# Performance work log

Hardware: AMD Instinct MI355X
Metric: run time of the kernel (lower is better)

## Reference

```python
import jax, jax.numpy as jnp
import numpy as np

ARITY, LABEL_DIM, H_DIM, B = 2, 128, 512, 16384
ARG_DIM = LABEL_DIM + ARITY * H_DIM


def setup_inputs() -> dict:
    key = jax.random.key(0)
    ks = jax.random.split(key, 12)
    s_lin = 1.0 / np.sqrt(ARG_DIM)
    inp = {
        "label": jax.random.normal(ks[0], (B, LABEL_DIM), jnp.float32),
        "children_h": jax.random.normal(ks[1], (ARITY, B, H_DIM), jnp.float32),
        "children_c": jax.random.normal(ks[2], (ARITY, B, H_DIM), jnp.float32),
        # torch Linear params: W (h, arg_dim), b (h,)
        "W_i": jax.random.normal(ks[3], (H_DIM, ARG_DIM), jnp.float32) * s_lin,
        "b_i": jax.random.normal(ks[4], (H_DIM,), jnp.float32) * s_lin,
        "W_o": jax.random.normal(ks[5], (H_DIM, ARG_DIM), jnp.float32) * s_lin,
        "b_o": jax.random.normal(ks[6], (H_DIM,), jnp.float32) * s_lin,
        "W_u": jax.random.normal(ks[7], (H_DIM, ARG_DIM), jnp.float32) * s_lin,
        "b_u": jax.random.normal(ks[8], (H_DIM,), jnp.float32) * s_lin,
        # forget params (xavier-ish init)
        "W_fl": jax.random.normal(ks[9], (H_DIM, LABEL_DIM), jnp.float32) * np.sqrt(2.0 / (H_DIM + LABEL_DIM)),
        "W_fs": jax.random.normal(ks[10], (ARITY, ARITY, H_DIM, H_DIM), jnp.float32) * np.sqrt(1.0 / H_DIM),
        "forget_bias": jax.random.normal(ks[11], (H_DIM,), jnp.float32) * 0.1,
    }
    return inp


def reference(label, children_h, children_c, W_i, b_i, W_o, b_o, W_u, b_u, W_fl, W_fs, forget_bias):
    arity, b, h = children_h.shape
    # x = cat([label, h_0, ..., h_{arity-1}], dim=1)  -> (B, arg_dim)
    x = jnp.concatenate([label, children_h.transpose(1, 0, 2).reshape(b, arity * h)], axis=1)
    i_gate = jax.nn.sigmoid(x @ W_i.T + b_i)
    o_gate = jax.nn.sigmoid(x @ W_o.T + b_o)
    u = jnp.tanh(x @ W_u.T + b_u)
    # per-child forget weight: [W_fl | W_fs[k,0] | ... | W_fs[k,arity-1]]  -> (arity, h, arg_dim)
    Wf = jnp.concatenate(
        [jnp.broadcast_to(W_fl, (arity,) + W_fl.shape),
         W_fs.transpose(0, 2, 1, 3).reshape(arity, h, arity * h)],
        axis=2,
    )
    # bmm (no bias inside sigmoid; forget_bias enters separately below)
    f = jax.nn.sigmoid(jnp.einsum("khd,bd->kbh", Wf, x))
    cells_composed = (f * children_c).sum(axis=0)          # (B, h)
    cells_forget_bias = forget_bias * children_c.sum(axis=0)
    next_cell = i_gate * u + cells_composed + cells_forget_bias
    out = jnp.tanh(o_gate * next_cell)
    return (next_cell, out)
```

## Files before the change

kernel.cpp:

```cpp
#include <hip/hip_runtime.h>
#include <hip/hip_bf16.h>
#include <cstdint>
#include <cstddef>

#define BROWS   16384
#define LDIM    128
#define HDIM    512
#define KDIM    1152
#define NGATES  2560
#define NKT     (KDIM / 64)

#define XB_BYTES  ((size_t)BROWS * KDIM * 2)
#define WB_BYTES  ((size_t)NGATES * KDIM * 2)

using f32x4   = __attribute__((ext_vector_type(4))) float;
using bfrag   = __attribute__((ext_vector_type(8))) short;

__device__ __forceinline__ short f2bf(float f) {
    union { float f; uint32_t u; } a; a.f = f;
    uint32_t u = a.u;
    uint32_t lsb = (u >> 16) & 1u;
    u += 0x7fffu + lsb;
    return (short)(u >> 16);
}
__device__ __forceinline__ float bf2f(short s) {
    union { uint32_t u; float f; } a;
    a.u = ((uint32_t)(uint16_t)s) << 16;
    return a.f;
}

__device__ __forceinline__ void load_lds16(const void* g, void* l) {
    __builtin_amdgcn_global_load_lds(
        (const __attribute__((address_space(1))) void*)g,
        (__attribute__((address_space(3))) void*)l, 16, 0, 0);
}

__device__ __forceinline__ float fast_sigmoid(float x) {
    return 1.0f / (1.0f + __expf(-x));
}
__device__ __forceinline__ float fast_tanh(float x) {
    float t = __expf(2.0f * x);
    return 1.0f - 2.0f / (t + 1.0f);
}

#define NBX  ((BROWS  * (KDIM / 8)) / 256)
#define NBW  ((NGATES * (KDIM / 8)) / 256)

__global__ __launch_bounds__(256) void pack_all(
    const float* __restrict__ label, const float* __restrict__ chh,
    const float* __restrict__ Wi, const float* __restrict__ Wo,
    const float* __restrict__ Wu, const float* __restrict__ Wfl,
    const float* __restrict__ Wfs,
    short* __restrict__ xb, short* __restrict__ Wb)
{
    const int perRow = KDIM / 8;
    int blk = blockIdx.x;
    const float* src;
    short* dst;
    if (blk < NBX) {
        int tid = blk * 256 + threadIdx.x;
        int b = tid / perRow;
        int d = (tid - b * perRow) * 8;
        if (d < LDIM) {
            src = label + (size_t)b * LDIM + d;
        } else {
            int dd = d - LDIM;
            int k  = dd >> 9;
            int j  = dd & 511;
            src = chh + ((size_t)k * BROWS + b) * HDIM + j;
        }
        dst = xb + (size_t)b * KDIM + d;
    } else {
        int tid = (blk - NBX) * 256 + threadIdx.x;
        int n = tid / perRow;
        int d = (tid - n * perRow) * 8;
        int g = n >> 9, h = n & 511;
        if (g == 0)      src = Wi + (size_t)h * KDIM + d;
        else if (g == 1) src = Wo + (size_t)h * KDIM + d;
        else if (g == 2) src = Wu + (size_t)h * KDIM + d;
        else {
            int k = g - 3;
            if (d < LDIM) {
                src = Wfl + (size_t)h * LDIM + d;
            } else {
                int dd = d - LDIM;
                int j  = dd >> 9;
                int jj = dd & 511;
                src = Wfs + (((size_t)(k * 2 + j) * HDIM + h) * HDIM) + jj;
            }
        }
        dst = Wb + (size_t)n * KDIM + d;
    }
    float4 v0 = *(const float4*)src;
    float4 v1 = *(const float4*)(src + 4);
    bfrag s;
    s[0] = f2bf(v0.x); s[1] = f2bf(v0.y); s[2] = f2bf(v0.z); s[3] = f2bf(v0.w);
    s[4] = f2bf(v1.x); s[5] = f2bf(v1.y); s[6] = f2bf(v1.z); s[7] = f2bf(v1.w);
    *(bfrag*)dst = s;
}

__global__ __launch_bounds__(512, 2) void gemm_bt(const short* __restrict__ A,
                                                  const short* __restrict__ Bt,
                                                  short* __restrict__ C) {
    __shared__ short As[2][16384];
    __shared__ short Bs[2][16384];

    const int t    = threadIdx.x;
    const int lane = t & 63;
    const int wave = t >> 6;
    const int wr   = wave >> 2;
    const int wc   = wave & 3;
    const int quad = lane >> 4;
    const int l16  = lane & 15;

    const int local = blockIdx.x >> 3;
    const int mT    = (blockIdx.x & 7) * 8 + local / 10;
    const int nT    = local % 10;
    const int mBase = mT * 256;
    const int nBase = nT * 256;

    f32x4 acc[8][4] = {};

    const int sr  = t >> 3;
    const int ssl = (t & 7) ^ (sr & 7);
    const short* aSrc = A  + (size_t)(mBase + sr) * KDIM + ssl * 8;
    const short* bSrc = Bt + (size_t)(nBase + sr) * KDIM + ssl * 8;
    short* aDst = &As[0][0] + t * 8;
    short* bDst = &Bs[0][0] + t * 8;

#define STAGE_A(q, kt, buf) load_lds16(aSrc + (size_t)(q) * (64 * KDIM) + (kt) * 64, \
                                       aDst + (buf) * 16384 + (q) * 4096)
#define STAGE_B(q, kt, buf) load_lds16(bSrc + (size_t)(q) * (64 * KDIM) + (kt) * 64, \
                                       bDst + (buf) * 16384 + (q) * 4096)

    const int kswz0 = ((quad)     ^ (l16 & 7)) << 4;
    const int kswz1 = ((quad + 4) ^ (l16 & 7)) << 4;
    const int aRowB = (wr * 128 + l16) << 7;
    const int bRowB = (wc * 64  + l16) << 7;

#define DS_A(buf, mh, i, ks) (*(const bfrag*)((const char*)(&As[(buf)][0]) + aRowB + \
                              (mh) * 8192 + (i) * 2048 + ((ks) ? kswz1 : kswz0)))
#define DS_B(buf, j, ks) (*(const bfrag*)((const char*)(&Bs[(buf)][0]) + bRowB + \
                              (j) * 2048 + ((ks) ? kswz1 : kswz0)))

#define MM(af, bfr, mi, ni) acc[mi][ni] = \
    __builtin_amdgcn_mfma_f32_16x16x32_bf16(af, bfr, acc[mi][ni], 0, 0, 0)

#define PHASE(buf, mh, ks, ...) do { \
    bfrag a0 = DS_A(buf, mh, 0, ks); \
    bfrag a1 = DS_A(buf, mh, 1, ks); \
    bfrag a2 = DS_A(buf, mh, 2, ks); \
    bfrag a3 = DS_A(buf, mh, 3, ks); \
    bfrag b0 = DS_B(buf, 0, ks); \
    bfrag b1 = DS_B(buf, 1, ks); \
    bfrag b2 = DS_B(buf, 2, ks); \
    bfrag b3 = DS_B(buf, 3, ks); \
    __VA_ARGS__; \
    __builtin_amdgcn_s_setprio(1); \
    MM(a0, b0, (mh)*4+0, 0); MM(a0, b1, (mh)*4+0, 1); \
    MM(a0, b2, (mh)*4+0, 2); MM(a0, b3, (mh)*4+0, 3); \
    MM(a1, b0, (mh)*4+1, 0); MM(a1, b1, (mh)*4+1, 1); \
    MM(a1, b2, (mh)*4+1, 2); MM(a1, b3, (mh)*4+1, 3); \
    MM(a2, b0, (mh)*4+2, 0); MM(a2, b1, (mh)*4+2, 1); \
    MM(a2, b2, (mh)*4+2, 2); MM(a2, b3, (mh)*4+2, 3); \
    MM(a3, b0, (mh)*4+3, 0); MM(a3, b1, (mh)*4+3, 1); \
    MM(a3, b2, (mh)*4+3, 2); MM(a3, b3, (mh)*4+3, 3); \
    __builtin_amdgcn_s_setprio(0); \
} while (0)

    STAGE_A(0, 0, 0); STAGE_A(1, 0, 0); STAGE_A(2, 0, 0); STAGE_A(3, 0, 0);
    STAGE_B(0, 0, 0); STAGE_B(1, 0, 0); STAGE_B(2, 0, 0); STAGE_B(3, 0, 0);
    STAGE_A(0, 1, 1); STAGE_A(2, 1, 1);
    asm volatile("s_waitcnt vmcnt(2)" ::: "memory");
    __builtin_amdgcn_s_barrier();

#pragma unroll 1
    for (int k2 = 0; k2 < NKT / 2; ++k2) {
        const int kt   = 2 * k2;
        const bool more = (k2 < NKT / 2 - 1);

        PHASE(0, 0, 0, STAGE_A(1, kt + 1, 1); STAGE_B(0, kt + 1, 1); STAGE_B(1, kt + 1, 1));
        __builtin_amdgcn_s_barrier();
        PHASE(0, 0, 1, STAGE_A(3, kt + 1, 1); STAGE_B(2, kt + 1, 1); STAGE_B(3, kt + 1, 1));
        __builtin_amdgcn_s_barrier();
        PHASE(0, 1, 0, if (more) STAGE_A(0, kt + 2, 0));
        __builtin_amdgcn_s_barrier();
        PHASE(0, 1, 1, if (more) STAGE_A(2, kt + 2, 0));
        if (more) { asm volatile("s_waitcnt vmcnt(2)" ::: "memory"); }
        else      { asm volatile("s_waitcnt vmcnt(0)" ::: "memory"); }
        __builtin_amdgcn_s_barrier();

        PHASE(1, 0, 0, if (more) { STAGE_A(1, kt + 2, 0); STAGE_B(0, kt + 2, 0); STAGE_B(1, kt + 2, 0); });
        __builtin_amdgcn_s_barrier();
        PHASE(1, 0, 1, if (more) { STAGE_A(3, kt + 2, 0); STAGE_B(2, kt + 2, 0); STAGE_B(3, kt + 2, 0); });
        __builtin_amdgcn_s_barrier();
        PHASE(1, 1, 0, if (more) STAGE_A(0, kt + 3, 1));
        __builtin_amdgcn_s_barrier();
        PHASE(1, 1, 1, if (more) STAGE_A(2, kt + 3, 1));
        if (more) { asm volatile("s_waitcnt vmcnt(2)" ::: "memory"); }
        else      { asm volatile("s_waitcnt vmcnt(0)" ::: "memory"); }
        __builtin_amdgcn_s_barrier();
    }

#pragma unroll
    for (int mi = 0; mi < 8; ++mi) {
        const int row0 = mBase + wr * 128 + mi * 16 + quad * 4;
#pragma unroll
        for (int ni = 0; ni < 4; ++ni) {
            const int col = nBase + wc * 64 + ni * 16 + l16;
#pragma unroll
            for (int r = 0; r < 4; ++r) {
                C[(size_t)(row0 + r) * NGATES + col] = f2bf(acc[mi][ni][r]);
            }
        }
    }
#undef PHASE
#undef MM
#undef DS_A
#undef DS_B
#undef STAGE_A
#undef STAGE_B
}

__global__ __launch_bounds__(256) void epilogue(const short* __restrict__ gates,
                                                const float* __restrict__ chc,
                                                const float* __restrict__ b_i,
                                                const float* __restrict__ b_o,
                                                const float* __restrict__ b_u,
                                                const float* __restrict__ fbias,
                                                float* __restrict__ out) {
    int tid = blockIdx.x * 256 + threadIdx.x;
    int b  = tid >> 6;
    int h8 = (tid & 63) << 3;

    const short* g = gates + (size_t)b * NGATES + h8;
    bfrag vi  = *(const bfrag*)(g);
    bfrag vo  = *(const bfrag*)(g + HDIM);
    bfrag vu  = *(const bfrag*)(g + 2 * HDIM);
    bfrag vf0 = *(const bfrag*)(g + 3 * HDIM);
    bfrag vf1 = *(const bfrag*)(g + 4 * HDIM);

    float4 bi0 = *(const float4*)(b_i + h8),   bi1 = *(const float4*)(b_i + h8 + 4);
    float4 bo0 = *(const float4*)(b_o + h8),   bo1 = *(const float4*)(b_o + h8 + 4);
    float4 bu0 = *(const float4*)(b_u + h8),   bu1 = *(const float4*)(b_u + h8 + 4);
    float4 fb0 = *(const float4*)(fbias + h8), fb1 = *(const float4*)(fbias + h8 + 4);

    size_t cbase = (size_t)b * HDIM + h8;
    float4 c00 = *(const float4*)(chc + cbase);
    float4 c01 = *(const float4*)(chc + cbase + 4);
    float4 c10 = *(const float4*)(chc + (size_t)BROWS * HDIM + cbase);
    float4 c11 = *(const float4*)(chc + (size_t)BROWS * HDIM + cbase + 4);

    float bi[8] = {bi0.x,bi0.y,bi0.z,bi0.w, bi1.x,bi1.y,bi1.z,bi1.w};
    float bo[8] = {bo0.x,bo0.y,bo0.z,bo0.w, bo1.x,bo1.y,bo1.z,bo1.w};
    float bu[8] = {bu0.x,bu0.y,bu0.z,bu0.w, bu1.x,bu1.y,bu1.z,bu1.w};
    float fb[8] = {fb0.x,fb0.y,fb0.z,fb0.w, fb1.x,fb1.y,fb1.z,fb1.w};
    float c0[8] = {c00.x,c00.y,c00.z,c00.w, c01.x,c01.y,c01.z,c01.w};
    float c1[8] = {c10.x,c10.y,c10.z,c10.w, c11.x,c11.y,c11.z,c11.w};

    float nc[8], ou[8];
#pragma unroll
    for (int e = 0; e < 8; ++e) {
        float ig = fast_sigmoid(bf2f(vi[e]) + bi[e]);
        float og = fast_sigmoid(bf2f(vo[e]) + bo[e]);
        float uu = fast_tanh(bf2f(vu[e]) + bu[e]);
        float f0 = fast_sigmoid(bf2f(vf0[e]));
        float f1 = fast_sigmoid(bf2f(vf1[e]));
        float ncell = ig * uu + f0 * c0[e] + f1 * c1[e] + fb[e] * (c0[e] + c1[e]);
        nc[e] = ncell;
        ou[e] = fast_tanh(og * ncell);
    }
    float4 n0 = {nc[0], nc[1], nc[2], nc[3]}, n1 = {nc[4], nc[5], nc[6], nc[7]};
    float4 o0 = {ou[0], ou[1], ou[2], ou[3]}, o1 = {ou[4], ou[5], ou[6], ou[7]};
    *(float4*)(out + cbase)     = n0;
    *(float4*)(out + cbase + 4) = n1;
    *(float4*)(out + (size_t)BROWS * HDIM + cbase)     = o0;
    *(float4*)(out + (size_t)BROWS * HDIM + cbase + 4) = o1;
}

extern "C" void kernel_launch(void* const* d_in, const int* in_sizes, int n_in,
                              void* d_out, int out_size, void* d_ws, size_t ws_size,
                              hipStream_t stream) {
    const float* label = (const float*)d_in[0];
    const float* chh   = (const float*)d_in[1];
    const float* chc   = (const float*)d_in[2];
    const float* W_i   = (const float*)d_in[3];
    const float* b_i   = (const float*)d_in[4];
    const float* W_o   = (const float*)d_in[5];
    const float* b_o   = (const float*)d_in[6];
    const float* W_u   = (const float*)d_in[7];
    const float* b_u   = (const float*)d_in[8];
    const float* W_fl  = (const float*)d_in[9];
    const float* W_fs  = (const float*)d_in[10];
    const float* fbias = (const float*)d_in[11];
    float* out = (float*)d_out;

    char* ws = (char*)d_ws;
    short* xb    = (short*)ws;
    short* Wb    = (short*)(ws + XB_BYTES);
    short* gates = (short*)(ws + XB_BYTES + WB_BYTES);

    pack_all<<<NBX + NBW, 256, 0, stream>>>(label, chh, W_i, W_o, W_u, W_fl, W_fs, xb, Wb);

    gemm_bt<<<dim3(640), 512, 0, stream>>>(xb, Wb, gates);

    epilogue<<<(BROWS * (HDIM / 8)) / 256, 256, 0, stream>>>(gates, chc, b_i, b_o, b_u, fbias, out);
}
```

Measured before the change: 332.2 us.

## Switch GEMM main loop to triple-buffered K=32 tiles with single barrier per tile

The bf16 GEMM main loop now uses 32-wide K tiles held in a three-stage LDS ring instead of 64-wide tiles in a double buffer. Each tile issues the prefetch two tiles ahead, loads all A/B fragments, runs 32 MFMAs, then waits and syncs once. This cuts the number of barriers per K step and deepens prefetch to hide global-load latency. The cost is more loop iterations with less MFMA work between each sync, and a different LDS swizzle pattern.

```diff
diff --git a/kernel.cpp b/kernel.cpp
--- a/kernel.cpp
+++ b/kernel.cpp
@@ -8,7 +8,7 @@
 #define HDIM    512
 #define KDIM    1152
 #define NGATES  2560
-#define NKT     (KDIM / 64)
+#define NKT32   36
 
 #define XB_BYTES  ((size_t)BROWS * KDIM * 2)
 #define WB_BYTES  ((size_t)NGATES * KDIM * 2)
@@ -102,8 +102,8 @@
 __global__ __launch_bounds__(512, 2) void gemm_bt(const short* __restrict__ A,
                                                   const short* __restrict__ Bt,
                                                   short* __restrict__ C) {
-    __shared__ short As[2][16384];
-    __shared__ short Bs[2][16384];
+    __shared__ short As[3][8192];
+    __shared__ short Bs[3][8192];
 
     const int t    = threadIdx.x;
     const int lane = t & 63;
@@ -121,100 +121,76 @@
 
     f32x4 acc[8][4] = {};
 
-    const int sr  = t >> 3;
-    const int ssl = (t & 7) ^ (sr & 7);
+    const int sr  = t >> 2;
+    const int ssl = (t & 3) ^ (sr & 3);
     const short* aSrc = A  + (size_t)(mBase + sr) * KDIM + ssl * 8;
     const short* bSrc = Bt + (size_t)(nBase + sr) * KDIM + ssl * 8;
     short* aDst = &As[0][0] + t * 8;
     short* bDst = &Bs[0][0] + t * 8;
 
-#define STAGE_A(q, kt, buf) load_lds16(aSrc + (size_t)(q) * (64 * KDIM) + (kt) * 64, \
-                                       aDst + (buf) * 16384 + (q) * 4096)
-#define STAGE_B(q, kt, buf) load_lds16(bSrc + (size_t)(q) * (64 * KDIM) + (kt) * 64, \
-                                       bDst + (buf) * 16384 + (q) * 4096)
-
-    const int kswz0 = ((quad)     ^ (l16 & 7)) << 4;
-    const int kswz1 = ((quad + 4) ^ (l16 & 7)) << 4;
-    const int aRowB = (wr * 128 + l16) << 7;
-    const int bRowB = (wc * 64  + l16) << 7;
-
-#define DS_A(buf, mh, i, ks) (*(const bfrag*)((const char*)(&As[(buf)][0]) + aRowB + \
-                              (mh) * 8192 + (i) * 2048 + ((ks) ? kswz1 : kswz0)))
-#define DS_B(buf, j, ks) (*(const bfrag*)((const char*)(&Bs[(buf)][0]) + bRowB + \
-                              (j) * 2048 + ((ks) ? kswz1 : kswz0)))
-
-#define MM(af, bfr, mi, ni) acc[mi][ni] = \
-    __builtin_amdgcn_mfma_f32_16x16x32_bf16(af, bfr, acc[mi][ni], 0, 0, 0)
-
-#define PHASE(buf, mh, ks, ...) do { \
-    bfrag a0 = DS_A(buf, mh, 0, ks); \
-    bfrag a1 = DS_A(buf, mh, 1, ks); \
-    bfrag a2 = DS_A(buf, mh, 2, ks); \
-    bfrag a3 = DS_A(buf, mh, 3, ks); \
-    bfrag b0 = DS_B(buf, 0, ks); \
-    bfrag b1 = DS_B(buf, 1, ks); \
-    bfrag b2 = DS_B(buf, 2, ks); \
-    bfrag b3 = DS_B(buf, 3, ks); \
-    __VA_ARGS__; \
+#define STAGE_A(d, kt, buf) load_lds16(aSrc + (size_t)(d) * (128 * KDIM) + (kt) * 32, \
+                                       aDst + (buf) * 8192 + (d) * 4096)
+#define STAGE_B(d, kt, buf) load_lds16(bSrc + (size_t)(d) * (128 * KDIM) + (kt) * 32, \
+                                       bDst + (buf) * 8192 + (d) * 4096)
+
+    const int kswz  = (quad ^ (l16 & 3)) << 4;
+    const int aRowB = (wr * 128 + l16) * 64;
+    const int bRowB = (wc * 64  + l16) * 64;
+
+#define DS_A(buf, i) (*(const bfrag*)((const char*)(&As[0][0]) + (buf) * 16384 + aRowB + (i) * 1024 + kswz))
+#define DS_B(buf, j) (*(const bfrag*)((const char*)(&Bs[0][0]) + (buf) * 16384 + bRowB + (j) * 1024 + kswz))
+
+#define MM(af, bfr, i, j) acc[i][j] = \
+    __builtin_amdgcn_mfma_f32_16x16x32_bf16(af, bfr, acc[i][j], 0, 0, 0)
+
+#define TILE(bufc, bufs, kt, doStage, vmZero) do { \
+    if (doStage) { STAGE_A(0, (kt) + 2, bufs); STAGE_A(1, (kt) + 2, bufs); \
+                   STAGE_B(0, (kt) + 2, bufs); STAGE_B(1, (kt) + 2, bufs); } \
+    bfrag bb[4], aa[8]; \
+    bb[0] = DS_B(bufc, 0); bb[1] = DS_B(bufc, 1); \
+    bb[2] = DS_B(bufc, 2); bb[3] = DS_B(bufc, 3); \
+    aa[0] = DS_A(bufc, 0); aa[1] = DS_A(bufc, 1); \
+    aa[2] = DS_A(bufc, 2); aa[3] = DS_A(bufc, 3); \
+    aa[4] = DS_A(bufc, 4); aa[5] = DS_A(bufc, 5); \
+    aa[6] = DS_A(bufc, 6); aa[7] = DS_A(bufc, 7); \
     __builtin_amdgcn_s_setprio(1); \
-    MM(a0, b0, (mh)*4+0, 0); MM(a0, b1, (mh)*4+0, 1); \
-    MM(a0, b2, (mh)*4+0, 2); MM(a0, b3, (mh)*4+0, 3); \
-    MM(a1, b0, (mh)*4+1, 0); MM(a1, b1, (mh)*4+1, 1); \
-    MM(a1, b2, (mh)*4+1, 2); MM(a1, b3, (mh)*4+1, 3); \
-    MM(a2, b0, (mh)*4+2, 0); MM(a2, b1, (mh)*4+2, 1); \
-    MM(a2, b2, (mh)*4+2, 2); MM(a2, b3, (mh)*4+2, 3); \
-    MM(a3, b0, (mh)*4+3, 0); MM(a3, b1, (mh)*4+3, 1); \
-    MM(a3, b2, (mh)*4+3, 2); MM(a3, b3, (mh)*4+3, 3); \
+    _Pragma("unroll") \
+    for (int i = 0; i < 8; ++i) { \
+        _Pragma("unroll") \
+        for (int j = 0; j < 4; ++j) MM(aa[i], bb[j], i, j); \
+    } \
     __builtin_amdgcn_s_setprio(0); \
+    if (vmZero) { asm volatile("s_waitcnt vmcnt(0)" ::: "memory"); } \
+    else        { asm volatile("s_waitcnt vmcnt(4)" ::: "memory"); } \
+    __builtin_amdgcn_s_barrier(); \
 } while (0)
 
-    STAGE_A(0, 0, 0); STAGE_A(1, 0, 0); STAGE_A(2, 0, 0); STAGE_A(3, 0, 0);
-    STAGE_B(0, 0, 0); STAGE_B(1, 0, 0); STAGE_B(2, 0, 0); STAGE_B(3, 0, 0);
-    STAGE_A(0, 1, 1); STAGE_A(2, 1, 1);
-    asm volatile("s_waitcnt vmcnt(2)" ::: "memory");
+    STAGE_A(0, 0, 0); STAGE_A(1, 0, 0); STAGE_B(0, 0, 0); STAGE_B(1, 0, 0);
+    STAGE_A(0, 1, 1); STAGE_A(1, 1, 1); STAGE_B(0, 1, 1); STAGE_B(1, 1, 1);
+    asm volatile("s_waitcnt vmcnt(4)" ::: "memory");
     __builtin_amdgcn_s_barrier();
 
 #pragma unroll 1
-    for (int k2 = 0; k2 < NKT / 2; ++k2) {
-        const int kt   = 2 * k2;
-        const bool more = (k2 < NKT / 2 - 1);
-
-        PHASE(0, 0, 0, STAGE_A(1, kt + 1, 1); STAGE_B(0, kt + 1, 1); STAGE_B(1, kt + 1, 1));
-        __builtin_amdgcn_s_barrier();
-        PHASE(0, 0, 1, STAGE_A(3, kt + 1, 1); STAGE_B(2, kt + 1, 1); STAGE_B(3, kt + 1, 1));
-        __builtin_amdgcn_s_barrier();
-        PHASE(0, 1, 0, if (more) STAGE_A(0, kt + 2, 0));
-        __builtin_amdgcn_s_barrier();
-        PHASE(0, 1, 1, if (more) STAGE_A(2, kt + 2, 0));
-        if (more) { asm volatile("s_waitcnt vmcnt(2)" ::: "memory"); }
-        else      { asm volatile("s_waitcnt vmcnt(0)" ::: "memory"); }
-        __builtin_amdgcn_s_barrier();
-
-        PHASE(1, 0, 0, if (more) { STAGE_A(1, kt + 2, 0); STAGE_B(0, kt + 2, 0); STAGE_B(1, kt + 2, 0); });
-        __builtin_amdgcn_s_barrier();
-        PHASE(1, 0, 1, if (more) { STAGE_A(3, kt + 2, 0); STAGE_B(2, kt + 2, 0); STAGE_B(3, kt + 2, 0); });
-        __builtin_amdgcn_s_barrier();
-        PHASE(1, 1, 0, if (more) STAGE_A(0, kt + 3, 1));
-        __builtin_amdgcn_s_barrier();
-        PHASE(1, 1, 1, if (more) STAGE_A(2, kt + 3, 1));
-        if (more) { asm volatile("s_waitcnt vmcnt(2)" ::: "memory"); }
-        else      { asm volatile("s_waitcnt vmcnt(0)" ::: "memory"); }
-        __builtin_amdgcn_s_barrier();
-    }
-
-#pragma unroll
-    for (int mi = 0; mi < 8; ++mi) {
-        const int row0 = mBase + wr * 128 + mi * 16 + quad * 4;
-#pragma unroll
-        for (int ni = 0; ni < 4; ++ni) {
-            const int col = nBase + wc * 64 + ni * 16 + l16;
+    for (int k3 = 0; k3 < NKT32 / 3; ++k3) {
+        const int kt = k3 * 3;
+        TILE(0, 2, kt,     kt + 2 <= NKT32 - 1, false);
+        TILE(1, 0, kt + 1, kt + 3 <= NKT32 - 1, kt + 1 == NKT32 - 2);
+        TILE(2, 1, kt + 2, kt + 4 <= NKT32 - 1, kt + 2 == NKT32 - 2);
+    }
+
+#pragma unroll
+    for (int i = 0; i < 8; ++i) {
+        const int row0 = mBase + wr * 128 + i * 16 + quad * 4;
+#pragma unroll
+        for (int j = 0; j < 4; ++j) {
+            const int col = nBase + wc * 64 + j * 16 + l16;
 #pragma unroll
             for (int r = 0; r < 4; ++r) {
-                C[(size_t)(row0 + r) * NGATES + col] = f2bf(acc[mi][ni][r]);
+                C[(size_t)(row0 + r) * NGATES + col] = f2bf(acc[i][j][r]);
             }
         }
     }
-#undef PHASE
+#undef TILE
 #undef MM
 #undef DS_A
 #undef DS_B
```

Result: no change. 337.1 us (+1.5%).

## Fuse LSTM gate epilogue into GEMM with per-h gate-grouped tiles

Applied to the files above, without the earlier changes.

Restructures the GEMM so each block computes all five gate columns for a 64-wide slice of hidden units, then applies the sigmoid/tanh cell update directly from accumulators. This removes the bf16 gates intermediate buffer, its global write and read, and the separate epilogue launch. In exchange LDS per block grows to hold a 320-row B tile, which may reduce occupancy. Epilogue global accesses become scalar and less coalesced.

```diff
diff --git a/kernel.cpp b/kernel.cpp
--- a/kernel.cpp
+++ b/kernel.cpp
@@ -22,11 +22,6 @@
     uint32_t lsb = (u >> 16) & 1u;
     u += 0x7fffu + lsb;
     return (short)(u >> 16);
-}
-__device__ __forceinline__ float bf2f(short s) {
-    union { uint32_t u; float f; } a;
-    a.u = ((uint32_t)(uint16_t)s) << 16;
-    return a.f;
 }
 
 __device__ __forceinline__ void load_lds16(const void* g, void* l) {
@@ -99,11 +94,15 @@
     *(bfrag*)dst = s;
 }
 
-__global__ __launch_bounds__(512, 2) void gemm_bt(const short* __restrict__ A,
-                                                  const short* __restrict__ Bt,
-                                                  short* __restrict__ C) {
+__global__ __launch_bounds__(512, 2) void gemm_fused(
+    const short* __restrict__ A, const short* __restrict__ Wb,
+    const float* __restrict__ chc,
+    const float* __restrict__ b_i, const float* __restrict__ b_o,
+    const float* __restrict__ b_u, const float* __restrict__ fbias,
+    float* __restrict__ out)
+{
     __shared__ short As[2][16384];
-    __shared__ short Bs[2][16384];
+    __shared__ short Bs[2][20480];
 
     const int t    = threadIdx.x;
     const int lane = t & 63;
@@ -114,37 +113,37 @@
     const int l16  = lane & 15;
 
     const int local = blockIdx.x >> 3;
-    const int mT    = (blockIdx.x & 7) * 8 + local / 10;
-    const int nT    = local % 10;
+    const int mT    = (blockIdx.x & 7) * 8 + (local >> 3);
+    const int nT    = local & 7;
     const int mBase = mT * 256;
-    const int nBase = nT * 256;
-
-    f32x4 acc[8][4] = {};
+    const int h0    = nT * 64;
+
+    f32x4 acc[8][5] = {};
 
     const int sr  = t >> 3;
     const int ssl = (t & 7) ^ (sr & 7);
     const short* aSrc = A  + (size_t)(mBase + sr) * KDIM + ssl * 8;
-    const short* bSrc = Bt + (size_t)(nBase + sr) * KDIM + ssl * 8;
+    const short* bSrc = Wb + (size_t)(h0    + sr) * KDIM + ssl * 8;
     short* aDst = &As[0][0] + t * 8;
     short* bDst = &Bs[0][0] + t * 8;
 
 #define STAGE_A(q, kt, buf) load_lds16(aSrc + (size_t)(q) * (64 * KDIM) + (kt) * 64, \
                                        aDst + (buf) * 16384 + (q) * 4096)
-#define STAGE_B(q, kt, buf) load_lds16(bSrc + (size_t)(q) * (64 * KDIM) + (kt) * 64, \
-                                       bDst + (buf) * 16384 + (q) * 4096)
+#define STAGE_B(d, kt, buf) load_lds16(bSrc + (size_t)(d) * (512 * KDIM) + (kt) * 64, \
+                                       bDst + (buf) * 20480 + (d) * 4096)
 
     const int kswz0 = ((quad)     ^ (l16 & 7)) << 4;
     const int kswz1 = ((quad + 4) ^ (l16 & 7)) << 4;
     const int aRowB = (wr * 128 + l16) << 7;
-    const int bRowB = (wc * 64  + l16) << 7;
-
-#define DS_A(buf, mh, i, ks) (*(const bfrag*)((const char*)(&As[(buf)][0]) + aRowB + \
-                              (mh) * 8192 + (i) * 2048 + ((ks) ? kswz1 : kswz0)))
-#define DS_B(buf, j, ks) (*(const bfrag*)((const char*)(&Bs[(buf)][0]) + bRowB + \
-                              (j) * 2048 + ((ks) ? kswz1 : kswz0)))
-
-#define MM(af, bfr, mi, ni) acc[mi][ni] = \
-    __builtin_amdgcn_mfma_f32_16x16x32_bf16(af, bfr, acc[mi][ni], 0, 0, 0)
+    const int bRowB = (wc * 16  + l16) << 7;
+
+#define DS_A(buf, mh, i, ks) (*(const bfrag*)((const char*)(&As[0][0]) + (buf) * 32768 + \
+                              aRowB + (mh) * 8192 + (i) * 2048 + ((ks) ? kswz1 : kswz0)))
+#define DS_B(buf, g, ks) (*(const bfrag*)((const char*)(&Bs[0][0]) + (buf) * 40960 + \
+                              (g) * 8192 + bRowB + ((ks) ? kswz1 : kswz0)))
+
+#define MM(af, bfr, mi, g) acc[mi][g] = \
+    __builtin_amdgcn_mfma_f32_16x16x32_bf16(af, bfr, acc[mi][g], 0, 0, 0)
 
 #define PHASE(buf, mh, ks, ...) do { \
     bfrag a0 = DS_A(buf, mh, 0, ks); \
@@ -155,21 +154,23 @@
     bfrag b1 = DS_B(buf, 1, ks); \
     bfrag b2 = DS_B(buf, 2, ks); \
     bfrag b3 = DS_B(buf, 3, ks); \
+    bfrag b4 = DS_B(buf, 4, ks); \
     __VA_ARGS__; \
     __builtin_amdgcn_s_setprio(1); \
-    MM(a0, b0, (mh)*4+0, 0); MM(a0, b1, (mh)*4+0, 1); \
-    MM(a0, b2, (mh)*4+0, 2); MM(a0, b3, (mh)*4+0, 3); \
-    MM(a1, b0, (mh)*4+1, 0); MM(a1, b1, (mh)*4+1, 1); \
-    MM(a1, b2, (mh)*4+1, 2); MM(a1, b3, (mh)*4+1, 3); \
-    MM(a2, b0, (mh)*4+2, 0); MM(a2, b1, (mh)*4+2, 1); \
-    MM(a2, b2, (mh)*4+2, 2); MM(a2, b3, (mh)*4+2, 3); \
-    MM(a3, b0, (mh)*4+3, 0); MM(a3, b1, (mh)*4+3, 1); \
-    MM(a3, b2, (mh)*4+3, 2); MM(a3, b3, (mh)*4+3, 3); \
+    MM(a0, b0, (mh)*4+0, 0); MM(a0, b1, (mh)*4+0, 1); MM(a0, b2, (mh)*4+0, 2); \
+    MM(a0, b3, (mh)*4+0, 3); MM(a0, b4, (mh)*4+0, 4); \
+    MM(a1, b0, (mh)*4+1, 0); MM(a1, b1, (mh)*4+1, 1); MM(a1, b2, (mh)*4+1, 2); \
+    MM(a1, b3, (mh)*4+1, 3); MM(a1, b4, (mh)*4+1, 4); \
+    MM(a2, b0, (mh)*4+2, 0); MM(a2, b1, (mh)*4+2, 1); MM(a2, b2, (mh)*4+2, 2); \
+    MM(a2, b3, (mh)*4+2, 3); MM(a2, b4, (mh)*4+2, 4); \
+    MM(a3, b0, (mh)*4+3, 0); MM(a3, b1, (mh)*4+3, 1); MM(a3, b2, (mh)*4+3, 2); \
+    MM(a3, b3, (mh)*4+3, 3); MM(a3, b4, (mh)*4+3, 4); \
     __builtin_amdgcn_s_setprio(0); \
 } while (0)
 
     STAGE_A(0, 0, 0); STAGE_A(1, 0, 0); STAGE_A(2, 0, 0); STAGE_A(3, 0, 0);
     STAGE_B(0, 0, 0); STAGE_B(1, 0, 0); STAGE_B(2, 0, 0); STAGE_B(3, 0, 0);
+    STAGE_B(4, 0, 0);
     STAGE_A(0, 1, 1); STAGE_A(2, 1, 1);
     asm volatile("s_waitcnt vmcnt(2)" ::: "memory");
     __builtin_amdgcn_s_barrier();
@@ -183,7 +184,7 @@
         __builtin_amdgcn_s_barrier();
         PHASE(0, 0, 1, STAGE_A(3, kt + 1, 1); STAGE_B(2, kt + 1, 1); STAGE_B(3, kt + 1, 1));
         __builtin_amdgcn_s_barrier();
-        PHASE(0, 1, 0, if (more) STAGE_A(0, kt + 2, 0));
+        PHASE(0, 1, 0, STAGE_B(4, kt + 1, 1); if (more) STAGE_A(0, kt + 2, 0));
         __builtin_amdgcn_s_barrier();
         PHASE(0, 1, 1, if (more) STAGE_A(2, kt + 2, 0));
         if (more) { asm volatile("s_waitcnt vmcnt(2)" ::: "memory"); }
@@ -194,24 +195,35 @@
         __builtin_amdgcn_s_barrier();
         PHASE(1, 0, 1, if (more) { STAGE_A(3, kt + 2, 0); STAGE_B(2, kt + 2, 0); STAGE_B(3, kt + 2, 0); });
         __builtin_amdgcn_s_barrier();
-        PHASE(1, 1, 0, if (more) STAGE_A(0, kt + 3, 1));
+        PHASE(1, 1, 0, if (more) { STAGE_B(4, kt + 2, 0); STAGE_A(0, kt + 3, 1); });
         __builtin_amdgcn_s_barrier();
         PHASE(1, 1, 1, if (more) STAGE_A(2, kt + 3, 1));
         if (more) { asm volatile("s_waitcnt vmcnt(2)" ::: "memory"); }
         else      { asm volatile("s_waitcnt vmcnt(0)" ::: "memory"); }
         __builtin_amdgcn_s_barrier();
     }
+
+    const int h = h0 + wc * 16 + l16;
+    const float bi = b_i[h], bo = b_o[h], bu = b_u[h], fb = fbias[h];
+    const float* chc1 = chc + (size_t)BROWS * HDIM;
+    float* out2 = out + (size_t)BROWS * HDIM;
 
 #pragma unroll
     for (int mi = 0; mi < 8; ++mi) {
         const int row0 = mBase + wr * 128 + mi * 16 + quad * 4;
 #pragma unroll
-        for (int ni = 0; ni < 4; ++ni) {
-            const int col = nBase + wc * 64 + ni * 16 + l16;
-#pragma unroll
-            for (int r = 0; r < 4; ++r) {
-                C[(size_t)(row0 + r) * NGATES + col] = f2bf(acc[mi][ni][r]);
-            }
+        for (int r = 0; r < 4; ++r) {
+            const size_t idx = (size_t)(row0 + r) * HDIM + h;
+            float ig = fast_sigmoid(acc[mi][0][r] + bi);
+            float og = fast_sigmoid(acc[mi][1][r] + bo);
+            float uu = fast_tanh(acc[mi][2][r] + bu);
+            float f0 = fast_sigmoid(acc[mi][3][r]);
+            float f1 = fast_sigmoid(acc[mi][4][r]);
+            float c0 = chc[idx];
+            float c1 = chc1[idx];
+            float ncell = ig * uu + f0 * c0 + f1 * c1 + fb * (c0 + c1);
+            out[idx]  = ncell;
+            out2[idx] = fast_tanh(og * ncell);
         }
     }
 #undef PHASE
@@ -220,62 +232,6 @@
 #undef DS_B
 #undef STAGE_A
 #undef STAGE_B
-}
-
-__global__ __launch_bounds__(256) void epilogue(const short* __restrict__ gates,
-                                                const float* __restrict__ chc,
-                                                const float* __restrict__ b_i,
-                                                const float* __restrict__ b_o,
-                                                const float* __restrict__ b_u,
-                                                const float* __restrict__ fbias,
-                                                float* __restrict__ out) {
-    int tid = blockIdx.x * 256 + threadIdx.x;
-    int b  = tid >> 6;
-    int h8 = (tid & 63) << 3;
-
-    const short* g = gates + (size_t)b * NGATES + h8;
-    bfrag vi  = *(const bfrag*)(g);
-    bfrag vo  = *(const bfrag*)(g + HDIM);
-    bfrag vu  = *(const bfrag*)(g + 2 * HDIM);
-    bfrag vf0 = *(const bfrag*)(g + 3 * HDIM);
-    bfrag vf1 = *(const bfrag*)(g + 4 * HDIM);
-
-    float4 bi0 = *(const float4*)(b_i + h8),   bi1 = *(const float4*)(b_i + h8 + 4);
-    float4 bo0 = *(const float4*)(b_o + h8),   bo1 = *(const float4*)(b_o + h8 + 4);
-    float4 bu0 = *(const float4*)(b_u + h8),   bu1 = *(const float4*)(b_u + h8 + 4);
-    float4 fb0 = *(const float4*)(fbias + h8), fb1 = *(const float4*)(fbias + h8 + 4);
-
-    size_t cbase = (size_t)b * HDIM + h8;
-    float4 c00 = *(const float4*)(chc + cbase);
-    float4 c01 = *(const float4*)(chc + cbase + 4);
-    float4 c10 = *(const float4*)(chc + (size_t)BROWS * HDIM + cbase);
-    float4 c11 = *(const float4*)(chc + (size_t)BROWS * HDIM + cbase + 4);
-
-    float bi[8] = {bi0.x,bi0.y,bi0.z,bi0.w, bi1.x,bi1.y,bi1.z,bi1.w};
-    float bo[8] = {bo0.x,bo0.y,bo0.z,bo0.w, bo1.x,bo1.y,bo1.z,bo1.w};
-    float bu[8] = {bu0.x,bu0.y,bu0.z,bu0.w, bu1.x,bu1.y,bu1.z,bu1.w};
-    float fb[8] = {fb0.x,fb0.y,fb0.z,fb0.w, fb1.x,fb1.y,fb1.z,fb1.w};
-    float c0[8] = {c00.x,c00.y,c00.z,c00.w, c01.x,c01.y,c01.z,c01.w};
-    float c1[8] = {c10.x,c10.y,c10.z,c10.w, c11.x,c11.y,c11.z,c11.w};
-
-    float nc[8], ou[8];
-#pragma unroll
-    for (int e = 0; e < 8; ++e) {
-        float ig = fast_sigmoid(bf2f(vi[e]) + bi[e]);
-        float og = fast_sigmoid(bf2f(vo[e]) + bo[e]);
-        float uu = fast_tanh(bf2f(vu[e]) + bu[e]);
-        float f0 = fast_sigmoid(bf2f(vf0[e]));
-        float f1 = fast_sigmoid(bf2f(vf1[e]));
-        float ncell = ig * uu + f0 * c0[e] + f1 * c1[e] + fb[e] * (c0[e] + c1[e]);
-        nc[e] = ncell;
-        ou[e] = fast_tanh(og * ncell);
-    }
-    float4 n0 = {nc[0], nc[1], nc[2], nc[3]}, n1 = {nc[4], nc[5], nc[6], nc[7]};
-    float4 o0 = {ou[0], ou[1], ou[2], ou[3]}, o1 = {ou[4], ou[5], ou[6], ou[7]};
-    *(float4*)(out + cbase)     = n0;
-    *(float4*)(out + cbase + 4) = n1;
-    *(float4*)(out + (size_t)BROWS * HDIM + cbase)     = o0;
-    *(float4*)(out + (size_t)BROWS * HDIM + cbase + 4) = o1;
 }
 
 extern "C" void kernel_launch(void* const* d_in, const int* in_sizes, int n_in,
@@ -296,13 +252,10 @@
     float* out = (float*)d_out;
 
     char* ws = (char*)d_ws;
-    short* xb    = (short*)ws;
-    short* Wb    = (short*)(ws + XB_BYTES);
-    short* gates = (short*)(ws + XB_BYTES + WB_BYTES);
+    short* xb = (short*)ws;
+    short* Wb = (short*)(ws + XB_BYTES);
 
     pack_all<<<NBX + NBW, 256, 0, stream>>>(label, chh, W_i, W_o, W_u, W_fl, W_fs, xb, Wb);
 
-    gemm_bt<<<dim3(640), 512, 0, stream>>>(xb, Wb, gates);
-
-    epilogue<<<(BROWS * (HDIM / 8)) / 256, 256, 0, stream>>>(gates, chc, b_i, b_o, b_u, fbias, out);
-}
+    gemm_fused<<<dim3(512), 512, 0, stream>>>(xb, Wb, chc, b_i, b_o, b_u, fbias, out);
+}
```

Measured after the change: 295.7 us. -11.0%, faster.
